# Kernel optimization log

Hardware: AMD Instinct MI355X
Metric: run time of the kernel (lower is better)

Reference implementation:

```python
import jax, jax.numpy as jnp
import numpy as np

N_NODES = 50000
N_EDGES = 800000
NODE_DIM = 128
HIDDEN = 128
N_LAYERS = 2
EPS = 1e-5


def _layer_norm(h, gamma, beta):
    mu = jnp.mean(h, axis=-1, keepdims=True)
    var = jnp.mean(jnp.square(h - mu), axis=-1, keepdims=True)
    return (h - mu) * jax.lax.rsqrt(var + EPS) * gamma + beta


def setup_inputs() -> dict:
    key = jax.random.key(0)
    ks = jax.random.split(key, 12)
    s = 0.05  # small init scale for numerical sanity
    x = jax.random.normal(ks[0], (N_NODES, NODE_DIM), jnp.float32)
    edge_index = jax.random.randint(ks[1], (2, N_EDGES), 0, N_NODES, dtype=jnp.int64)
    # node_encoder: Linear(node_dim -> hidden)
    W_enc = jax.random.normal(ks[2], (HIDDEN, NODE_DIM), jnp.float32) * s
    b_enc = jnp.zeros((HIDDEN,), jnp.float32)
    # per-layer params, stacked over layers (L leading dim)
    Wm1 = jax.random.normal(ks[3], (N_LAYERS, HIDDEN, 2 * HIDDEN), jnp.float32) * s
    bm1 = jnp.zeros((N_LAYERS, HIDDEN), jnp.float32)
    Wm2 = jax.random.normal(ks[4], (N_LAYERS, HIDDEN, HIDDEN), jnp.float32) * s
    bm2 = jnp.zeros((N_LAYERS, HIDDEN), jnp.float32)
    Wu = jax.random.normal(ks[5], (N_LAYERS, HIDDEN, 2 * HIDDEN), jnp.float32) * s
    bu = jnp.zeros((N_LAYERS, HIDDEN), jnp.float32)
    gamma = jnp.ones((N_LAYERS, HIDDEN), jnp.float32)
    beta = jnp.zeros((N_LAYERS, HIDDEN), jnp.float32)
    # output_proj: Linear(hidden -> hidden)
    W_out = jax.random.normal(ks[6], (HIDDEN, HIDDEN), jnp.float32) * s
    b_out = jnp.zeros((HIDDEN,), jnp.float32)
    return {
        "x": x, "edge_index": edge_index,
        "W_enc": W_enc, "b_enc": b_enc,
        "Wm1": Wm1, "bm1": bm1, "Wm2": Wm2, "bm2": bm2,
        "Wu": Wu, "bu": bu, "gamma": gamma, "beta": beta,
        "W_out": W_out, "b_out": b_out,
    }


def reference(x, edge_index, W_enc, b_enc, Wm1, bm1, Wm2, bm2, Wu, bu, gamma, beta, W_out, b_out):
    row, col = edge_index[0], edge_index[1]
    h = x @ W_enc.T + b_enc  # [N, H]
    for l in range(N_LAYERS):
        # gather -> concat -> message MLP  ([E, 2H] -> [E, H])
        m = jnp.concatenate([h[row], h[col]], axis=-1)
        m = jax.nn.relu(m @ Wm1[l].T + bm1[l])
        m = m @ Wm2[l].T + bm2[l]
        # scatter_add over destination nodes (col)
        agg = jax.ops.segment_sum(m, col, num_segments=N_NODES)  # [N, H]
        upd = jnp.concatenate([h, agg], axis=-1) @ Wu[l].T + bu[l]
        h = _layer_norm(h + upd, gamma[l], beta[l])
    return h @ W_out.T + b_out  # node_embeddings [N, H]
```

## Files before the change

kernel.cpp:

```cpp
#include <hip/hip_runtime.h>

#define N_NODES 50000
#define N_EDGES 800000
#define HID 128
#define EPS 1e-5f
#define NBKT 782
#define ESLICE 3125
#define NSLICE 256

typedef __attribute__((ext_vector_type(8))) short s16x8;
typedef __attribute__((ext_vector_type(4))) float f32x4;
typedef __attribute__((ext_vector_type(4))) int i32x4;

__device__ __forceinline__ unsigned short f2bf(float f) {
  unsigned int u = __float_as_uint(f);
  u += 0x7fffu + ((u >> 16) & 1u);
  return (unsigned short)(u >> 16);
}
__device__ __forceinline__ unsigned int pack2(float a, float b) {
  return (unsigned int)f2bf(a) | ((unsigned int)f2bf(b) << 16);
}
__device__ __forceinline__ float bflo(unsigned int u) { return __uint_as_float(u << 16); }
__device__ __forceinline__ float bfhi(unsigned int u) { return __uint_as_float(u & 0xffff0000u); }
__device__ __forceinline__ float bf2f(unsigned short u) { return __uint_as_float((unsigned int)u << 16); }

__global__ __launch_bounds__(256) void prep_hist_kernel(
    const float* __restrict__ W_enc, const float* __restrict__ W_out,
    const float* __restrict__ Wm1, const float* __restrict__ Wu,
    const float* __restrict__ Wm2, const float* __restrict__ bm2,
    unsigned int* __restrict__ Wenc_b, unsigned int* __restrict__ Wout_b,
    unsigned int* __restrict__ Wpq_b, unsigned short* __restrict__ Wcat_b,
    float* __restrict__ bfold, const int* __restrict__ ei, int* __restrict__ shist) {
  __shared__ int lhist[NBKT];
  const int b = blockIdx.x, t = threadIdx.x;
  if (b >= 449) {
    const int sl = b - 449;
    const int e0 = sl * ESLICE;
    for (int i = t; i < NBKT; i += 256) lhist[i] = 0;
    __syncthreads();
    for (int e = e0 + t; e < e0 + ESLICE; e += 256)
      atomicAdd(&lhist[ei[N_EDGES + e] >> 6], 1);
    __syncthreads();
    for (int i = t; i < NBKT; i += 256) shist[sl * NBKT + i] = lhist[i];
    return;
  }
  if (b < 32) {
    int i = b * 256 + t;
    Wenc_b[i] = pack2(W_enc[2 * i], W_enc[2 * i + 1]);
  } else if (b < 64) {
    int i = (b - 32) * 256 + t;
    Wout_b[i] = pack2(W_out[2 * i], W_out[2 * i + 1]);
  } else if (b < 192) {
    int i = (b - 64) * 256 + t;
    int k2 = i & 63;
    int c = (i >> 6) & 255;
    int l = i >> 14;
    const float* srow = Wm1 + ((size_t)l * 128 + (c & 127)) * 256 + ((c >> 7) << 7);
    Wpq_b[i] = pack2(srow[2 * k2], srow[2 * k2 + 1]);
  } else if (b < 448) {
    int i = (b - 192) * 256 + t;
    int k = i & 255, c = (i >> 8) & 127, l = i >> 15;
    const float* wrow = Wu + ((size_t)l * 128 + c) * 256;
    float v;
    if (k < 128) {
      v = wrow[k];
    } else {
      const float* wb = wrow + 128;
      const float* m2 = Wm2 + (size_t)l * 128 * 128 + (k - 128);
      float s = 0.f;
      for (int j = 0; j < 128; ++j) s += wb[j] * m2[(size_t)j * 128];
      v = s;
    }
    Wcat_b[i] = f2bf(v);
  } else {
    int l = t >> 7, c = t & 127;
    const float* wb = Wu + ((size_t)l * 128 + c) * 256 + 128;
    const float* bv = bm2 + l * 128;
    float s = 0.f;
    for (int j = 0; j < 128; ++j) s += wb[j] * bv[j];
    bfold[t] = s;
  }
}

__global__ __launch_bounds__(256) void colsum_kernel(const int* __restrict__ shist,
                                                     int* __restrict__ bcounts) {
  int b = blockIdx.x * 256 + threadIdx.x;
  if (b >= NBKT) return;
  int s = 0;
  for (int j = 0; j < NSLICE; ++j) s += shist[j * NBKT + b];
  bcounts[b] = s;
}

__global__ __launch_bounds__(1024) void bscan_kernel(const int* __restrict__ bcounts,
                                                     int* __restrict__ boff,
                                                     int* __restrict__ bcursor) {
  __shared__ int wtot[16];
  const int t = threadIdx.x, lane = t & 63, w = t >> 6;
  int v = (t < NBKT) ? bcounts[t] : 0;
  int s = v;
#pragma unroll
  for (int off = 1; off < 64; off <<= 1) {
    int tt = __shfl_up(s, off);
    if (lane >= off) s += tt;
  }
  if (lane == 63) wtot[w] = s;
  __syncthreads();
  int woff = 0;
#pragma unroll
  for (int j = 0; j < 16; ++j) { int tv = wtot[j]; if (j < w) woff += tv; }
  int excl = woff + (s - v);
  if (t < NBKT) { boff[t] = excl; bcursor[t] = excl; }
  if (t == NBKT) boff[NBKT] = excl;
}

struct BscatSmem {
  int lhist[784], lstart[784], lcur[784], gbase[784];
  unsigned int staged[ESLICE];
  int wtot[4];
};
struct Sort64Smem { int hist[64]; int lcur[64]; };

__device__ __forceinline__ void bscatter_dev(BscatSmem& sm, const int* ei, int* bcursor,
                                             unsigned int* ebuf, int bx) {
  const int t = threadIdx.x, lane = t & 63, w = t >> 6;
  const int e0 = bx * ESLICE;

  for (int i = t; i < 784; i += 256) sm.lhist[i] = 0;
  __syncthreads();
  for (int e = e0 + t; e < e0 + ESLICE; e += 256)
    atomicAdd(&sm.lhist[ei[N_EDGES + e] >> 6], 1);
  __syncthreads();

  int tsum = 0;
  if (t < 196)
    tsum = sm.lhist[4 * t] + sm.lhist[4 * t + 1] + sm.lhist[4 * t + 2] + sm.lhist[4 * t + 3];
  int inc = tsum;
#pragma unroll
  for (int off = 1; off < 64; off <<= 1) {
    int tt = __shfl_up(inc, off);
    if (lane >= off) inc += tt;
  }
  if (lane == 63) sm.wtot[w] = inc;
  __syncthreads();
  int woff = 0;
#pragma unroll
  for (int j = 0; j < 4; ++j) { int tv = sm.wtot[j]; if (j < w) woff += tv; }
  if (t < 196) {
    int run = woff + inc - tsum;
#pragma unroll
    for (int j = 0; j < 4; ++j) {
      sm.lstart[4 * t + j] = run;
      sm.lcur[4 * t + j] = run;
      run += sm.lhist[4 * t + j];
    }
  }
  for (int bk = t; bk < NBKT; bk += 256)
    sm.gbase[bk] = sm.lhist[bk] ? atomicAdd(&bcursor[bk], sm.lhist[bk]) : 0;
  __syncthreads();

  for (int e = e0 + t; e < e0 + ESLICE; e += 256) {
    int s = ei[e], d = ei[N_EDGES + e];
    int pos = atomicAdd(&sm.lcur[d >> 6], 1);
    sm.staged[pos] = (unsigned int)s | ((unsigned int)(d & 63) << 16) |
                     ((unsigned int)(d >> 6) << 22);
  }
  __syncthreads();

  for (int i = t; i < ESLICE; i += 256) {
    unsigned int pk = sm.staged[i];
    int bk = pk >> 22;
    ebuf[sm.gbase[bk] + (i - sm.lstart[bk])] = pk;
  }
}

__device__ __forceinline__ void sort64_dev(Sort64Smem& sm, const unsigned int* ebuf,
                                           const int* boff, unsigned short* esrc,
                                           int* noff, int* counts, int b) {
  const int t = threadIdx.x;
  const int e0 = boff[b], e1 = boff[b + 1];
  if (t < 64) sm.hist[t] = 0;
  __syncthreads();
  for (int e = e0 + t; e < e1; e += 256)
    atomicAdd(&sm.hist[(ebuf[e] >> 16) & 63], 1);
  __syncthreads();
  if (t < 64) {
    int v = sm.hist[t];
    int s = v;
#pragma unroll
    for (int off = 1; off < 64; off <<= 1) {
      int tt = __shfl_up(s, off);
      if (t >= off) s += tt;
    }
    sm.lcur[t] = s - v;
    int node = b * 64 + t;
    if (node < N_NODES) {
      noff[node] = e0 + s - v;
      counts[node] = v;
    }
  }
  __syncthreads();
  for (int e = e0 + t; e < e1; e += 256) {
    unsigned int pk = ebuf[e];
    int pos = atomicAdd(&sm.lcur[(pk >> 16) & 63], 1);
    esrc[e0 + pos] = (unsigned short)(pk & 0xffffu);
  }
  if (b == NBKT - 1 && t == 0) noff[N_NODES] = e1;
}

template <int KS, bool AF32, bool DUAL, int MODE>
__device__ __forceinline__ void gemm3_dev(
    short* Bs, int bx, int gx, int by,
    const void* A0v, const unsigned short* A1,
    const unsigned short* W, const float* bias,
    const int* deg, const float* bias2,
    const float* gamma, const float* beta,
    const unsigned short* hres, float* outF,
    unsigned short* outB, int outw) {
  constexpr int KW = KS * 32;
  constexpr int NFRAG = KS * 8;
  const int lane = threadIdx.x & 63;
  const int w = threadIdx.x >> 6;
  const int cl = lane & 15;
  const int kb = (lane >> 4) * 8;
  const int co = by * 128;
  W += (size_t)by * 128 * KW;

  for (int f = w; f < NFRAG; f += 4) {
    int nt = f & 7, ks = f >> 3;
    s16x8 bv = *(const s16x8*)(W + (size_t)(nt * 16 + cl) * KW + ks * 32 + kb);
    *(s16x8*)(Bs + f * 512 + lane * 8) = bv;
  }
  __syncthreads();

  s16x8 breg[KS][8];
#pragma unroll
  for (int ks = 0; ks < KS; ++ks)
#pragma unroll
    for (int nt = 0; nt < 8; ++nt)
      breg[ks][nt] = *(const s16x8*)(Bs + (ks * 8 + nt) * 512 + lane * 8);

  float bs[8], b2[8], gs[8], bes[8];
#pragma unroll
  for (int nt = 0; nt < 8; ++nt) {
    int col = nt * 16 + cl;
    bs[nt] = bias ? bias[col] : 0.f;
    if constexpr (MODE == 2) {
      b2[nt] = bias2[col];
      gs[nt] = gamma[col];
      bes[nt] = beta[col];
    }
  }

  const int step = gx * 4;
  for (int rt = bx * 4 + w; rt < 3125; rt += step) {
    const int arow = rt * 16 + cl;
    f32x4 acc[8];
#pragma unroll
    for (int i = 0; i < 8; ++i) acc[i] = (f32x4){0.f, 0.f, 0.f, 0.f};
#pragma unroll
    for (int ks = 0; ks < KS; ++ks) {
      s16x8 a;
      if constexpr (AF32) {
        const float* ap = (const float*)A0v + (size_t)arow * HID + ks * 32 + kb;
        float4 lo = *(const float4*)ap;
        float4 hi = *(const float4*)(ap + 4);
        i32x4 ai = {(int)pack2(lo.x, lo.y), (int)pack2(lo.z, lo.w),
                    (int)pack2(hi.x, hi.y), (int)pack2(hi.z, hi.w)};
        a = __builtin_bit_cast(s16x8, ai);
      } else if constexpr (DUAL) {
        const unsigned short* base = (ks < KS / 2) ? (const unsigned short*)A0v : A1;
        int kss = (ks < KS / 2) ? ks : ks - KS / 2;
        a = *(const s16x8*)(base + (size_t)arow * HID + kss * 32 + kb);
      } else {
        a = *(const s16x8*)((const unsigned short*)A0v + (size_t)arow * HID + ks * 32 + kb);
      }
#pragma unroll
      for (int nt = 0; nt < 8; ++nt)
        acc[nt] = __builtin_amdgcn_mfma_f32_16x16x32_bf16(a, breg[ks][nt], acc[nt], 0, 0, 0);
    }

    const int rbase = rt * 16 + (lane >> 4) * 4;
    if constexpr (MODE == 2) {
#pragma unroll
      for (int reg = 0; reg < 4; ++reg) {
        int row = rbase + reg;
        float dv = (float)deg[row];
        float v[8];
        float s = 0.f, s2 = 0.f;
#pragma unroll
        for (int nt = 0; nt < 8; ++nt) {
          float hv = bf2f(hres[(size_t)row * HID + nt * 16 + cl]);
          v[nt] = acc[nt][reg] + bs[nt] + dv * b2[nt] + hv;
          s += v[nt];
          s2 += v[nt] * v[nt];
        }
#pragma unroll
        for (int m = 1; m < 16; m <<= 1) {
          s += __shfl_xor(s, m);
          s2 += __shfl_xor(s2, m);
        }
        float mu = s * (1.f / 128.f);
        float var = s2 * (1.f / 128.f) - mu * mu;
        float inv = rsqrtf(var + EPS);
#pragma unroll
        for (int nt = 0; nt < 8; ++nt) {
          float o = (v[nt] - mu) * inv * gs[nt] + bes[nt];
          outB[(size_t)row * HID + nt * 16 + cl] = f2bf(o);
        }
      }
    } else {
#pragma unroll
      for (int reg = 0; reg < 4; ++reg) {
        int row = rbase + reg;
#pragma unroll
        for (int nt = 0; nt < 8; ++nt) {
          float vv = acc[nt][reg] + bs[nt];
          if constexpr (MODE == 0) outF[(size_t)row * outw + co + nt * 16 + cl] = vv;
          else outB[(size_t)row * outw + co + nt * 16 + cl] = f2bf(vv);
        }
      }
    }
  }
}

template <int KS, bool AF32, bool DUAL, int MODE>
__global__ __launch_bounds__(256, DUAL ? 1 : 2) void gemm3(
    const void* __restrict__ A0v, const unsigned short* __restrict__ A1,
    const unsigned short* __restrict__ W, const float* __restrict__ bias,
    const int* __restrict__ deg, const float* __restrict__ bias2,
    const float* __restrict__ gamma, const float* __restrict__ beta,
    const unsigned short* __restrict__ hres, float* __restrict__ outF,
    unsigned short* __restrict__ outB, int outw) {
  __shared__ short Bs[KS * 8 * 512];
  gemm3_dev<KS, AF32, DUAL, MODE>(Bs, blockIdx.x, gridDim.x, blockIdx.y, A0v, A1, W, bias,
                                  deg, bias2, gamma, beta, hres, outF, outB, outw);
}

union MergedSmem1 { BscatSmem b; short Bs[32 * 512]; };
__global__ __launch_bounds__(256, 2) void k_bscat_enc(
    const int* __restrict__ ei, int* __restrict__ bcursor, unsigned int* __restrict__ ebuf,
    const float* __restrict__ x, const unsigned short* __restrict__ Wenc,
    const float* __restrict__ b_enc, unsigned short* __restrict__ hb) {
  __shared__ MergedSmem1 sm;
  if (blockIdx.x < NSLICE) {
    bscatter_dev(sm.b, ei, bcursor, ebuf, blockIdx.x);
  } else {
    gemm3_dev<4, true, false, 1>(sm.Bs, blockIdx.x - NSLICE, 512, 0, x, nullptr, Wenc, b_enc,
                                 nullptr, nullptr, nullptr, nullptr, nullptr, nullptr, hb, HID);
  }
}

union MergedSmem2 { Sort64Smem s; short Bs[32 * 512]; };
__global__ __launch_bounds__(256, 2) void k_sort_pq(
    const unsigned int* __restrict__ ebuf, const int* __restrict__ boff,
    unsigned short* __restrict__ esrc, int* __restrict__ noff, int* __restrict__ counts,
    const unsigned short* __restrict__ hb, const unsigned short* __restrict__ Wpq,
    unsigned short* __restrict__ pq) {
  __shared__ MergedSmem2 sm;
  if (blockIdx.x < NBKT) {
    sort64_dev(sm.s, ebuf, boff, esrc, noff, counts, blockIdx.x);
  } else {
    int bb = blockIdx.x - NBKT;
    gemm3_dev<4, false, false, 1>(sm.Bs, bb & 511, 512, bb >> 9, hb, nullptr, Wpq, nullptr,
                                  nullptr, nullptr, nullptr, nullptr, nullptr, nullptr, pq, 256);
  }
}

__device__ __forceinline__ void acc8(float* acc, const float* qf, uint4 u) {
  acc[0] += fmaxf(bflo(u.x) + qf[0], 0.f);
  acc[1] += fmaxf(bfhi(u.x) + qf[1], 0.f);
  acc[2] += fmaxf(bflo(u.y) + qf[2], 0.f);
  acc[3] += fmaxf(bfhi(u.y) + qf[3], 0.f);
  acc[4] += fmaxf(bflo(u.z) + qf[4], 0.f);
  acc[5] += fmaxf(bfhi(u.z) + qf[5], 0.f);
  acc[6] += fmaxf(bflo(u.w) + qf[6], 0.f);
  acc[7] += fmaxf(bfhi(u.w) + qf[7], 0.f);
}

__global__ __launch_bounds__(256) void aggregate5_kernel(
    const uint4* __restrict__ pq4, const float* __restrict__ bm1,
    const int* __restrict__ noff, const unsigned short* __restrict__ esrc,
    uint4* __restrict__ rb4) {
  const int node = blockIdx.x * 4 + (threadIdx.x >> 6);
  const int lane = threadIdx.x & 63;
  const int l = lane & 15;
  const int eh = lane >> 4;
  uint4 qv = pq4[(size_t)node * 32 + 16 + l];
  float4 b0 = *(const float4*)(bm1 + 8 * l);
  float4 b1 = *(const float4*)(bm1 + 8 * l + 4);
  float qf[8] = {bflo(qv.x) + b0.x, bfhi(qv.x) + b0.y, bflo(qv.y) + b0.z, bfhi(qv.y) + b0.w,
                 bflo(qv.z) + b1.x, bfhi(qv.z) + b1.y, bflo(qv.w) + b1.z, bfhi(qv.w) + b1.w};
  float acc[8] = {0.f, 0.f, 0.f, 0.f, 0.f, 0.f, 0.f, 0.f};
  const int i0 = noff[node], i1 = noff[node + 1];
  const int nfull = (i1 - i0) >> 4;
  int idx = i0 + eh;
  for (int j = 0; j < nfull; ++j, idx += 16) {
    int s0 = esrc[idx], s1 = esrc[idx + 4], s2 = esrc[idx + 8], s3 = esrc[idx + 12];
    uint4 u0 = pq4[(size_t)s0 * 32 + l];
    uint4 u1 = pq4[(size_t)s1 * 32 + l];
    uint4 u2 = pq4[(size_t)s2 * 32 + l];
    uint4 u3 = pq4[(size_t)s3 * 32 + l];
    acc8(acc, qf, u0);
    acc8(acc, qf, u1);
    acc8(acc, qf, u2);
    acc8(acc, qf, u3);
  }
  while (idx < i1) {
    uint4 u = pq4[(size_t)esrc[idx] * 32 + l];
    acc8(acc, qf, u);
    idx += 4;
  }
#pragma unroll
  for (int j = 0; j < 8; ++j) {
    acc[j] += __shfl_xor(acc[j], 16);
    acc[j] += __shfl_xor(acc[j], 32);
  }
  if (lane < 16) {
    uint4 r;
    r.x = pack2(acc[0], acc[1]);
    r.y = pack2(acc[2], acc[3]);
    r.z = pack2(acc[4], acc[5]);
    r.w = pack2(acc[6], acc[7]);
    rb4[(size_t)node * 16 + l] = r;
  }
}

extern "C" void kernel_launch(void* const* d_in, const int* in_sizes, int n_in,
                              void* d_out, int out_size, void* d_ws, size_t ws_size,
                              hipStream_t stream) {
  const float* x     = (const float*)d_in[0];
  const int*   ei    = (const int*)d_in[1];
  const float* W_enc = (const float*)d_in[2];
  const float* b_enc = (const float*)d_in[3];
  const float* Wm1   = (const float*)d_in[4];
  const float* bm1   = (const float*)d_in[5];
  const float* Wm2   = (const float*)d_in[6];
  const float* bm2   = (const float*)d_in[7];
  const float* Wu    = (const float*)d_in[8];
  const float* bu    = (const float*)d_in[9];
  const float* gamma = (const float*)d_in[10];
  const float* beta  = (const float*)d_in[11];
  const float* W_out = (const float*)d_in[12];
  const float* b_out = (const float*)d_in[13];
  float* out = (float*)d_out;

  char* ws = (char*)d_ws;
  const size_t NBH = (size_t)N_NODES * HID * 2;

  unsigned short* hb = (unsigned short*)(ws);
  unsigned short* pq = (unsigned short*)(ws + NBH);
  unsigned short* rb = (unsigned short*)(ws + 3 * NBH);
  char* wp = ws + 4 * NBH;
  unsigned short* Wenc_b = (unsigned short*)wp;
  unsigned short* Wout_b = Wenc_b + 16384;
  unsigned short* Wpq_b  = Wout_b + 16384;
  unsigned short* Wcat_b = Wpq_b + 65536;
  float*          bfold  = (float*)(Wcat_b + 65536);
  int* counts  = (int*)(bfold + 256);
  int* noff    = counts + N_NODES;
  int* boff    = noff + N_NODES + 1;
  int* bcounts = boff + NBKT + 1;
  int* bcursor = bcounts + NBKT;
  unsigned short* esrc = (unsigned short*)(bcursor + NBKT);
  unsigned int* ebuf = (unsigned int*)(esrc + N_EDGES);
  int* shist = (int*)(ebuf + N_EDGES);

  prep_hist_kernel<<<449 + NSLICE, 256, 0, stream>>>(
      W_enc, W_out, Wm1, Wu, Wm2, bm2, (unsigned int*)Wenc_b, (unsigned int*)Wout_b,
      (unsigned int*)Wpq_b, Wcat_b, bfold, ei, shist);
  colsum_kernel<<<4, 256, 0, stream>>>(shist, bcounts);
  bscan_kernel<<<1, 1024, 0, stream>>>(bcounts, boff, bcursor);
  k_bscat_enc<<<NSLICE + 512, 256, 0, stream>>>(ei, bcursor, ebuf, x, Wenc_b, b_enc, hb);
  k_sort_pq<<<NBKT + 1024, 256, 0, stream>>>(ebuf, boff, esrc, noff, counts, hb, Wpq_b, pq);

  for (int l = 0; l < 2; ++l) {
    const unsigned short* Wcatl = Wcat_b + l * 32768;
    const float* bm1l = bm1 + l * HID;
    const float* bul  = bu + l * HID;
    const float* bfl  = bfold + l * HID;
    const float* gl   = gamma + l * HID;
    const float* bl   = beta + l * HID;

    aggregate5_kernel<<<12500, 256, 0, stream>>>((const uint4*)pq, bm1l, noff, esrc,
                                                 (uint4*)rb);
    gemm3<8, false, true, 2><<<256, 256, 0, stream>>>(
        hb, rb, Wcatl, bul, counts, bfl, gl, bl, hb, nullptr, hb, HID);
    if (l == 0)
      gemm3<4, false, false, 1><<<dim3(512, 2), 256, 0, stream>>>(
          hb, nullptr, Wpq_b + 32768, nullptr, nullptr, nullptr, nullptr, nullptr, nullptr,
          nullptr, pq, 256);
  }

  gemm3<4, false, false, 0><<<512, 256, 0, stream>>>(
      hb, nullptr, Wout_b, b_out, nullptr, nullptr, nullptr, nullptr, nullptr,
      out, nullptr, HID);
}
```

Baseline: 205.3 us.

## Store P/Q and aggregates column-blocked and split aggregation by channel group

The P/Q projection outputs and the aggregation result now use a channel-major layout: 16-channel blocks, each stored contiguously over all nodes. The new aggregation kernel assigns each block to one 16-channel group, so each block gathers a 32-byte slice per edge. The idea is to keep each channel group's gather working set small enough to stay in cache, at the cost of re-reading the edge indices and offsets once per group. Separately, the column-sum kernel is folded into the single-block scan, which saves a launch but makes the scan block do all 256 summation passes serially.

```diff
diff --git a/kernel.cpp b/kernel.cpp
--- a/kernel.cpp
+++ b/kernel.cpp
@@ -82,21 +82,14 @@
   }
 }
 
-__global__ __launch_bounds__(256) void colsum_kernel(const int* __restrict__ shist,
-                                                     int* __restrict__ bcounts) {
-  int b = blockIdx.x * 256 + threadIdx.x;
-  if (b >= NBKT) return;
-  int s = 0;
-  for (int j = 0; j < NSLICE; ++j) s += shist[j * NBKT + b];
-  bcounts[b] = s;
-}
-
-__global__ __launch_bounds__(1024) void bscan_kernel(const int* __restrict__ bcounts,
+__global__ __launch_bounds__(1024) void bscan_kernel(const int* __restrict__ shist,
                                                      int* __restrict__ boff,
                                                      int* __restrict__ bcursor) {
   __shared__ int wtot[16];
   const int t = threadIdx.x, lane = t & 63, w = t >> 6;
-  int v = (t < NBKT) ? bcounts[t] : 0;
+  int v = 0;
+  if (t < NBKT)
+    for (int j = 0; j < NSLICE; ++j) v += shist[j * NBKT + t];
   int s = v;
 #pragma unroll
   for (int off = 1; off < 64; off <<= 1) {
@@ -207,7 +200,7 @@
   if (b == NBKT - 1 && t == 0) noff[N_NODES] = e1;
 }
 
-template <int KS, bool AF32, bool DUAL, int MODE>
+template <int KS, bool AF32, bool DUAL, int MODE, bool CMOUT = false, bool A1CM = false>
 __device__ __forceinline__ void gemm3_dev(
     short* Bs, int bx, int gx, int by,
     const void* A0v, const unsigned short* A1,
@@ -268,9 +261,15 @@
                     (int)pack2(hi.x, hi.y), (int)pack2(hi.z, hi.w)};
         a = __builtin_bit_cast(s16x8, ai);
       } else if constexpr (DUAL) {
-        const unsigned short* base = (ks < KS / 2) ? (const unsigned short*)A0v : A1;
-        int kss = (ks < KS / 2) ? ks : ks - KS / 2;
-        a = *(const s16x8*)(base + (size_t)arow * HID + kss * 32 + kb);
+        if (ks < KS / 2) {
+          a = *(const s16x8*)((const unsigned short*)A0v + (size_t)arow * HID + ks * 32 + kb);
+        } else {
+          int kk = (ks - KS / 2) * 32 + kb;
+          if constexpr (A1CM)
+            a = *(const s16x8*)(A1 + ((size_t)(kk >> 4) * N_NODES + arow) * 16 + (kk & 15));
+          else
+            a = *(const s16x8*)(A1 + (size_t)arow * HID + kk);
+        }
       } else {
         a = *(const s16x8*)((const unsigned short*)A0v + (size_t)arow * HID + ks * 32 + kb);
       }
@@ -316,6 +315,8 @@
         for (int nt = 0; nt < 8; ++nt) {
           float vv = acc[nt][reg] + bs[nt];
           if constexpr (MODE == 0) outF[(size_t)row * outw + co + nt * 16 + cl] = vv;
+          else if constexpr (CMOUT)
+            outB[((size_t)(by * 8 + nt) * N_NODES + row) * 16 + cl] = f2bf(vv);
           else outB[(size_t)row * outw + co + nt * 16 + cl] = f2bf(vv);
         }
       }
@@ -323,7 +324,7 @@
   }
 }
 
-template <int KS, bool AF32, bool DUAL, int MODE>
+template <int KS, bool AF32, bool DUAL, int MODE, bool CMOUT = false, bool A1CM = false>
 __global__ __launch_bounds__(256, DUAL ? 1 : 2) void gemm3(
     const void* __restrict__ A0v, const unsigned short* __restrict__ A1,
     const unsigned short* __restrict__ W, const float* __restrict__ bias,
@@ -332,8 +333,9 @@
     const unsigned short* __restrict__ hres, float* __restrict__ outF,
     unsigned short* __restrict__ outB, int outw) {
   __shared__ short Bs[KS * 8 * 512];
-  gemm3_dev<KS, AF32, DUAL, MODE>(Bs, blockIdx.x, gridDim.x, blockIdx.y, A0v, A1, W, bias,
-                                  deg, bias2, gamma, beta, hres, outF, outB, outw);
+  gemm3_dev<KS, AF32, DUAL, MODE, CMOUT, A1CM>(Bs, blockIdx.x, gridDim.x, blockIdx.y, A0v,
+                                               A1, W, bias, deg, bias2, gamma, beta, hres,
+                                               outF, outB, outw);
 }
 
 union MergedSmem1 { BscatSmem b; short Bs[32 * 512]; };
@@ -361,67 +363,53 @@
     sort64_dev(sm.s, ebuf, boff, esrc, noff, counts, blockIdx.x);
   } else {
     int bb = blockIdx.x - NBKT;
-    gemm3_dev<4, false, false, 1>(sm.Bs, bb & 511, 512, bb >> 9, hb, nullptr, Wpq, nullptr,
-                                  nullptr, nullptr, nullptr, nullptr, nullptr, nullptr, pq, 256);
-  }
-}
-
-__device__ __forceinline__ void acc8(float* acc, const float* qf, uint4 u) {
-  acc[0] += fmaxf(bflo(u.x) + qf[0], 0.f);
-  acc[1] += fmaxf(bfhi(u.x) + qf[1], 0.f);
-  acc[2] += fmaxf(bflo(u.y) + qf[2], 0.f);
-  acc[3] += fmaxf(bfhi(u.y) + qf[3], 0.f);
-  acc[4] += fmaxf(bflo(u.z) + qf[4], 0.f);
-  acc[5] += fmaxf(bfhi(u.z) + qf[5], 0.f);
-  acc[6] += fmaxf(bflo(u.w) + qf[6], 0.f);
-  acc[7] += fmaxf(bfhi(u.w) + qf[7], 0.f);
-}
-
-__global__ __launch_bounds__(256) void aggregate5_kernel(
-    const uint4* __restrict__ pq4, const float* __restrict__ bm1,
+    gemm3_dev<4, false, false, 1, true>(sm.Bs, bb & 511, 512, bb >> 9, hb, nullptr, Wpq,
+                                        nullptr, nullptr, nullptr, nullptr, nullptr, nullptr,
+                                        nullptr, pq, 256);
+  }
+}
+
+__global__ __launch_bounds__(256) void aggregate6_kernel(
+    const unsigned int* __restrict__ pqcm,
+    const float* __restrict__ bm1,
     const int* __restrict__ noff, const unsigned short* __restrict__ esrc,
-    uint4* __restrict__ rb4) {
-  const int node = blockIdx.x * 4 + (threadIdx.x >> 6);
+    unsigned int* __restrict__ rbcm) {
+  const int cg = blockIdx.x & 7;
+  const int chunk = blockIdx.x >> 3;
   const int lane = threadIdx.x & 63;
-  const int l = lane & 15;
-  const int eh = lane >> 4;
-  uint4 qv = pq4[(size_t)node * 32 + 16 + l];
-  float4 b0 = *(const float4*)(bm1 + 8 * l);
-  float4 b1 = *(const float4*)(bm1 + 8 * l + 4);
-  float qf[8] = {bflo(qv.x) + b0.x, bfhi(qv.x) + b0.y, bflo(qv.y) + b0.z, bfhi(qv.y) + b0.w,
-                 bflo(qv.z) + b1.x, bfhi(qv.z) + b1.y, bflo(qv.w) + b1.z, bfhi(qv.w) + b1.w};
-  float acc[8] = {0.f, 0.f, 0.f, 0.f, 0.f, 0.f, 0.f, 0.f};
-  const int i0 = noff[node], i1 = noff[node + 1];
-  const int nfull = (i1 - i0) >> 4;
-  int idx = i0 + eh;
-  for (int j = 0; j < nfull; ++j, idx += 16) {
-    int s0 = esrc[idx], s1 = esrc[idx + 4], s2 = esrc[idx + 8], s3 = esrc[idx + 12];
-    uint4 u0 = pq4[(size_t)s0 * 32 + l];
-    uint4 u1 = pq4[(size_t)s1 * 32 + l];
-    uint4 u2 = pq4[(size_t)s2 * 32 + l];
-    uint4 u3 = pq4[(size_t)s3 * 32 + l];
-    acc8(acc, qf, u0);
-    acc8(acc, qf, u1);
-    acc8(acc, qf, u2);
-    acc8(acc, qf, u3);
-  }
-  while (idx < i1) {
-    uint4 u = pq4[(size_t)esrc[idx] * 32 + l];
-    acc8(acc, qf, u);
-    idx += 4;
-  }
-#pragma unroll
-  for (int j = 0; j < 8; ++j) {
-    acc[j] += __shfl_xor(acc[j], 16);
-    acc[j] += __shfl_xor(acc[j], 32);
-  }
-  if (lane < 16) {
-    uint4 r;
-    r.x = pack2(acc[0], acc[1]);
-    r.y = pack2(acc[2], acc[3]);
-    r.z = pack2(acc[4], acc[5]);
-    r.w = pack2(acc[6], acc[7]);
-    rb4[(size_t)node * 16 + l] = r;
+  const int w = threadIdx.x >> 6;
+  const int es = lane >> 3;
+  const int ch = lane & 7;
+  const unsigned int* pbase = pqcm + (size_t)cg * N_NODES * 8;
+  const unsigned int* qbase = pqcm + (size_t)(8 + cg) * N_NODES * 8;
+  unsigned int* rbase = rbcm + (size_t)cg * N_NODES * 8;
+  float2 bmv = *(const float2*)(bm1 + 2 * (cg * 8 + ch));
+  const int nbase = chunk * 16 + w * 4;
+#pragma unroll
+  for (int nn = 0; nn < 4; ++nn) {
+    const int node = nbase + nn;
+    unsigned int qv = qbase[(size_t)node * 8 + ch];
+    float q0 = bflo(qv) + bmv.x, q1 = bfhi(qv) + bmv.y;
+    float a0 = 0.f, a1 = 0.f;
+    const int i0 = noff[node], i1 = noff[node + 1];
+    int idx = i0 + es;
+    const int nfull = (i1 - i0) >> 3;
+    for (int j = 0; j < nfull; ++j, idx += 8) {
+      int src = esrc[idx];
+      unsigned int u = pbase[(size_t)src * 8 + ch];
+      a0 += fmaxf(bflo(u) + q0, 0.f);
+      a1 += fmaxf(bfhi(u) + q1, 0.f);
+    }
+    if (idx < i1) {
+      int src = esrc[idx];
+      unsigned int u = pbase[(size_t)src * 8 + ch];
+      a0 += fmaxf(bflo(u) + q0, 0.f);
+      a1 += fmaxf(bfhi(u) + q1, 0.f);
+    }
+    a0 += __shfl_xor(a0, 8);  a1 += __shfl_xor(a1, 8);
+    a0 += __shfl_xor(a0, 16); a1 += __shfl_xor(a1, 16);
+    a0 += __shfl_xor(a0, 32); a1 += __shfl_xor(a1, 32);
+    if (es == 0) rbase[(size_t)node * 8 + ch] = pack2(a0, a1);
   }
 }
 
@@ -459,8 +447,7 @@
   int* counts  = (int*)(bfold + 256);
   int* noff    = counts + N_NODES;
   int* boff    = noff + N_NODES + 1;
-  int* bcounts = boff + NBKT + 1;
-  int* bcursor = bcounts + NBKT;
+  int* bcursor = boff + NBKT + 1;
   unsigned short* esrc = (unsigned short*)(bcursor + NBKT);
   unsigned int* ebuf = (unsigned int*)(esrc + N_EDGES);
   int* shist = (int*)(ebuf + N_EDGES);
@@ -468,8 +455,7 @@
   prep_hist_kernel<<<449 + NSLICE, 256, 0, stream>>>(
       W_enc, W_out, Wm1, Wu, Wm2, bm2, (unsigned int*)Wenc_b, (unsigned int*)Wout_b,
       (unsigned int*)Wpq_b, Wcat_b, bfold, ei, shist);
-  colsum_kernel<<<4, 256, 0, stream>>>(shist, bcounts);
-  bscan_kernel<<<1, 1024, 0, stream>>>(bcounts, boff, bcursor);
+  bscan_kernel<<<1, 1024, 0, stream>>>(shist, boff, bcursor);
   k_bscat_enc<<<NSLICE + 512, 256, 0, stream>>>(ei, bcursor, ebuf, x, Wenc_b, b_enc, hb);
   k_sort_pq<<<NBKT + 1024, 256, 0, stream>>>(ebuf, boff, esrc, noff, counts, hb, Wpq_b, pq);
 
@@ -481,12 +467,12 @@
     const float* gl   = gamma + l * HID;
     const float* bl   = beta + l * HID;
 
-    aggregate5_kernel<<<12500, 256, 0, stream>>>((const uint4*)pq, bm1l, noff, esrc,
-                                                 (uint4*)rb);
-    gemm3<8, false, true, 2><<<256, 256, 0, stream>>>(
+    aggregate6_kernel<<<3125 * 8, 256, 0, stream>>>((const unsigned int*)pq, bm1l, noff,
+                                                    esrc, (unsigned int*)rb);
+    gemm3<8, false, true, 2, false, true><<<256, 256, 0, stream>>>(
         hb, rb, Wcatl, bul, counts, bfl, gl, bl, hb, nullptr, hb, HID);
     if (l == 0)
-      gemm3<4, false, false, 1><<<dim3(512, 2), 256, 0, stream>>>(
+      gemm3<4, false, false, 1, true><<<dim3(512, 2), 256, 0, stream>>>(
           hb, nullptr, Wpq_b + 32768, nullptr, nullptr, nullptr, nullptr, nullptr, nullptr,
           nullptr, pq, 256);
   }
```

Measured after the change: 297.6 us. 44.9% more time.
